# Performance work log

Measured on AMD Instinct MI355X. Metric: run time of the kernel, lower is better.

The kernel has to match this reference:

```python
import jax, jax.numpy as jnp
import numpy as np

T, D, H, E, K = 8192, 1024, 1024, 8, 2
N = T * K  # total dispatched rows


def setup_inputs() -> dict:
    key = jax.random.key(0)
    ks = jax.random.split(key, 12)
    s = 1.0 / np.sqrt(D)
    inp = {
        # uniform, contiguous per-expert segments: 2048 rows each
        'offsets': jnp.arange(E + 1, dtype=jnp.int64 if jax.config.jax_enable_x64 else jnp.int32) * (N // E),
        'jagged': jax.random.normal(ks[0], (T, D), jnp.float32),
        'weight': jax.random.normal(ks[1], (E, D, H), jnp.float32) * s,
        'bias': jax.random.normal(ks[2], (E, H), jnp.float32) * 0.02,
        'index': jax.random.randint(ks[3], (N,), 0, T),
        'weight_p': jax.random.normal(ks[4], (E, D, H), jnp.float32) * s,
        'weight_out': jax.random.normal(ks[5], (E, H, D), jnp.float32) * (1.0 / np.sqrt(H)),
        'reverse_index': jax.random.randint(ks[6], (T, K), 0, N),
        'gates': jax.random.uniform(ks[7], (N,), jnp.float32),
        'gates_index': jax.random.randint(ks[8], (T, K), 0, N),
        'bias_p': jax.random.normal(ks[9], (E, H), jnp.float32) * 0.02,
        'bias_out': jax.random.normal(ks[10], (E, D), jnp.float32) * 0.02,
    }
    return inp


def reference(offsets, jagged, weight, bias, index, weight_p, weight_out,
              reverse_index, gates, gates_index, bias_p, bias_out):
    # dispatch: gather token features into expert-sorted order  [N, D]
    x = jagged[index]
    n = x.shape[0]
    n_experts = weight.shape[0]
    # contiguous segment id per dispatched row
    expert_id = jnp.searchsorted(offsets, jnp.arange(n), side='right') - 1
    y = jnp.zeros((n, weight_out.shape[-1]), dtype=x.dtype)
    for e in range(n_experts):  # fixed small expert count
        m = (expert_id == e)[:, None].astype(x.dtype)
        xe = x * m
        g = xe @ weight[e] + bias[e]        # gate proj  [N, H]
        u = xe @ weight_p[e] + bias_p[e]    # up proj    [N, H]
        h = jax.nn.silu(g) * u              # SwiGLU
        y = y + (h @ weight_out[e] + bias_out[e]) * m
    # combine: gather K expert outputs per token, weight by gates  [T, D]
    gathered = y[reverse_index]             # [T, K, D]
    gv = gates[gates_index]                 # [T, K]
    return jnp.einsum('tkd,tk->td', gathered, gv)
```

## Files before the change

### kernel.cpp

```cpp
#include <hip/hip_runtime.h>
#include <hip/hip_bf16.h>

#define T_TOK 8192
#define DDIM 1024
#define HDIM 1024
#define NEXP 8
#define KTOP 2
#define NROWS (T_TOK * KTOP)

typedef __attribute__((ext_vector_type(8))) short bf16x8;
typedef __attribute__((ext_vector_type(8))) unsigned short u16x8;
typedef __attribute__((ext_vector_type(4))) float f32x4;

__device__ __forceinline__ unsigned short f2bf(float f) {
    unsigned u = __builtin_bit_cast(unsigned, f);
    u += 0x7fffu + ((u >> 16) & 1u);
    return (unsigned short)(u >> 16);
}
__device__ __forceinline__ float bf2f(unsigned short h) {
    return __builtin_bit_cast(float, (unsigned)h << 16);
}

__device__ __forceinline__ void gll16(const unsigned short* g, const unsigned short* l) {
    __builtin_amdgcn_global_load_lds(
        (const __attribute__((address_space(1))) unsigned int*)g,
        (__attribute__((address_space(3))) unsigned int*)l, 16, 0, 0);
}


__global__ __launch_bounds__(256) void cvt_bf16_k(const float* __restrict__ in,
                                                  unsigned short* __restrict__ out, int n4) {
    int i = blockIdx.x * 256 + threadIdx.x;
    if (i >= n4) return;
    float4 v = ((const float4*)in)[i];
    ushort4 o;
    o.x = f2bf(v.x); o.y = f2bf(v.y); o.z = f2bf(v.z); o.w = f2bf(v.w);
    ((ushort4*)out)[i] = o;
}

__global__ __launch_bounds__(256) void transpose_cast3_k(
    const float* __restrict__ w1, const float* __restrict__ w2,
    const float* __restrict__ w3, unsigned short* __restrict__ o1,
    unsigned short* __restrict__ o2, unsigned short* __restrict__ o3) {
    __shared__ float tile[64][65];
    int z = blockIdx.z;
    int which = z >> 3, m = z & 7;
    const float* src = (which == 0 ? w1 : which == 1 ? w2 : w3) + (size_t)m * DDIM * HDIM;
    unsigned short* dst = (which == 0 ? o1 : which == 1 ? o2 : o3) + (size_t)m * DDIM * HDIM;
    int c0 = blockIdx.x * 64, r0 = blockIdx.y * 64;
    int t = threadIdx.x;
    int rr = t >> 4;
    int cc = (t & 15) * 4;
#pragma unroll
    for (int p = 0; p < 4; ++p) {
        float4 v = *(const float4*)&src[(size_t)(r0 + rr + p * 16) * HDIM + c0 + cc];
        tile[rr + p * 16][cc]     = v.x;
        tile[rr + p * 16][cc + 1] = v.y;
        tile[rr + p * 16][cc + 2] = v.z;
        tile[rr + p * 16][cc + 3] = v.w;
    }
    __syncthreads();
    int rb = (t & 7) * 8;
    int oc = t >> 3;
#pragma unroll
    for (int q = 0; q < 2; ++q) {
        int c = oc + q * 32;
        u16x8 o;
#pragma unroll
        for (int j = 0; j < 8; ++j)
            o[j] = f2bf(tile[rb + j][c]);
        *(u16x8*)&dst[(size_t)(c0 + c) * DDIM + r0 + rb] = o;
    }
}


constexpr int BMk = 128, BNk = 128, BKk = 64;

template <int VARIANT>
__global__ __launch_bounds__(256, 4) void gemm128_k(
    const unsigned short* __restrict__ A, const int* __restrict__ rowidx, int lda,
    const unsigned short* __restrict__ Bt, const float* __restrict__ biasE,
    const unsigned short* __restrict__ Gin, unsigned short* __restrict__ Out,
    const int* __restrict__ offsets, int N, int K) {
    __shared__ __attribute__((aligned(16))) unsigned short lds[16384];

    const int nbn = N / BNk;
    int l = (blockIdx.x & 7) * 128 + (blockIdx.x >> 3);
    int brow = l / nbn, bcol = l % nbn;
    int row0 = brow * BMk, col0 = bcol * BNk;
    int e = 0;
    while (offsets[e + 1] <= row0) ++e;

    const unsigned short* Bte = Bt + (size_t)e * N * K;
    const float* bias = biasE + (size_t)e * N;

    int tid = threadIdx.x;
    int lane = tid & 63, wid = tid >> 6;
    int wr = wid >> 1, wc = wid & 1;
    int l15 = lane & 15, l4 = lane >> 4;

    int srow = lane >> 3;
    int c8 = ((lane & 7) ^ srow) * 8;
    const unsigned short* aS[4];
    const unsigned short* bS[4];
#pragma unroll
    for (int q = 0; q < 4; ++q) {
        int g = wid * 4 + q;
        int gr = row0 + g * 8 + srow;
        int ar = rowidx ? rowidx[gr] : gr;
        aS[q] = A + (size_t)ar * lda + c8;
        bS[q] = Bte + (size_t)(col0 + g * 8 + srow) * K + c8;
    }

    const char* LB = (const char*)lds;
    int arow = (wr * 64 + l15) * 128;
    int brw = (wc * 64 + l15) * 128;
    int cx = l15 & 7;
    int ch0 = (l4 ^ cx) * 16;
    int ch1 = ((4 + l4) ^ cx) * 16;

    f32x4 acc[4][4] = {};

#pragma unroll 1
    for (int t = 0; t < K / BKk; ++t) {
        int k0 = t * BKk;
#pragma unroll
        for (int q = 0; q < 4; ++q) {
            gll16(aS[q] + k0, lds + (wid * 4 + q) * 512);
            gll16(bS[q] + k0, lds + 8192 + (wid * 4 + q) * 512);
        }
        __syncthreads();
        bf16x8 fa[2][4], fb[2][4];
#pragma unroll
        for (int mi = 0; mi < 4; ++mi) {
            fa[0][mi] = *(const bf16x8*)(LB + arow + mi * 2048 + ch0);
            fa[1][mi] = *(const bf16x8*)(LB + arow + mi * 2048 + ch1);
        }
#pragma unroll
        for (int ni = 0; ni < 4; ++ni) {
            fb[0][ni] = *(const bf16x8*)(LB + 16384 + brw + ni * 2048 + ch0);
            fb[1][ni] = *(const bf16x8*)(LB + 16384 + brw + ni * 2048 + ch1);
        }
#pragma unroll
        for (int s = 0; s < 2; ++s)
#pragma unroll
            for (int mi = 0; mi < 4; ++mi)
#pragma unroll
                for (int ni = 0; ni < 4; ++ni)
                    acc[mi][ni] = __builtin_amdgcn_mfma_f32_16x16x32_bf16(
                        fa[s][mi], fb[s][ni], acc[mi][ni], 0, 0, 0);
        __syncthreads();
    }

    float bv[4];
#pragma unroll
    for (int ni = 0; ni < 4; ++ni)
        bv[ni] = bias[col0 + wc * 64 + ni * 16 + l15];

#pragma unroll
    for (int mi = 0; mi < 4; ++mi) {
        int orow_b = row0 + wr * 64 + mi * 16 + l4 * 4;
#pragma unroll
        for (int ni = 0; ni < 4; ++ni) {
            int ocol = col0 + wc * 64 + ni * 16 + l15;
#pragma unroll
            for (int q = 0; q < 4; ++q) {
                size_t oidx = (size_t)(orow_b + q) * N + ocol;
                float v = acc[mi][ni][q] + bv[ni];
                if (VARIANT == 1) {
                    float g = bf2f(Gin[oidx]);
                    float s = g / (1.0f + __expf(-g));
                    v = s * v;
                }
                Out[oidx] = f2bf(v);
            }
        }
    }
}


__global__ __launch_bounds__(256) void combine_k(
    const unsigned short* __restrict__ Y, const int* __restrict__ rev,
    const float* __restrict__ gates, const int* __restrict__ gidx,
    float* __restrict__ out) {
    int t = blockIdx.x;
    int r0 = rev[2 * t], r1 = rev[2 * t + 1];
    float g0 = gates[gidx[2 * t]], g1 = gates[gidx[2 * t + 1]];
    const unsigned short* y0 = Y + (size_t)r0 * DDIM;
    const unsigned short* y1 = Y + (size_t)r1 * DDIM;
    int d = threadIdx.x * 4;
    ushort4 a = *(const ushort4*)(y0 + d);
    ushort4 b = *(const ushort4*)(y1 + d);
    float4 r;
    r.x = g0 * bf2f(a.x) + g1 * bf2f(b.x);
    r.y = g0 * bf2f(a.y) + g1 * bf2f(b.y);
    r.z = g0 * bf2f(a.z) + g1 * bf2f(b.z);
    r.w = g0 * bf2f(a.w) + g1 * bf2f(b.w);
    *(float4*)(out + (size_t)t * DDIM + d) = r;
}


extern "C" void kernel_launch(void* const* d_in, const int* in_sizes, int n_in,
                              void* d_out, int out_size, void* d_ws, size_t ws_size,
                              hipStream_t stream) {
    const int* offsets = (const int*)d_in[0];
    const float* jagged = (const float*)d_in[1];
    const float* weight = (const float*)d_in[2];
    const float* bias = (const float*)d_in[3];
    const int* index = (const int*)d_in[4];
    const float* weight_p = (const float*)d_in[5];
    const float* weight_out = (const float*)d_in[6];
    const int* rev = (const int*)d_in[7];
    const float* gates = (const float*)d_in[8];
    const int* gidx = (const int*)d_in[9];
    const float* bias_p = (const float*)d_in[10];
    const float* bias_out = (const float*)d_in[11];
    float* out = (float*)d_out;

    char* w = (char*)d_ws;
    unsigned short* jag_bf = (unsigned short*)w; w += (size_t)T_TOK * DDIM * 2;
    unsigned short* W1t    = (unsigned short*)w; w += (size_t)NEXP * DDIM * HDIM * 2;
    unsigned short* Wpt    = (unsigned short*)w; w += (size_t)NEXP * DDIM * HDIM * 2;
    unsigned short* Wot    = (unsigned short*)w; w += (size_t)NEXP * HDIM * DDIM * 2;
    unsigned short* g_ws   = (unsigned short*)w; w += (size_t)NROWS * HDIM * 2;
    unsigned short* h_ws   = (unsigned short*)w; w += (size_t)NROWS * HDIM * 2;
    unsigned short* y_ws   = g_ws;

    cvt_bf16_k<<<(T_TOK * DDIM / 4 + 255) / 256, 256, 0, stream>>>(jagged, jag_bf, T_TOK * DDIM / 4);
    transpose_cast3_k<<<dim3(HDIM / 64, DDIM / 64, 3 * NEXP), 256, 0, stream>>>(
        weight, weight_p, weight_out, W1t, Wpt, Wot);

    const int grid = (NROWS / BMk) * (HDIM / BNk);

    gemm128_k<0><<<grid, 256, 0, stream>>>(jag_bf, index, DDIM, W1t, bias, nullptr, g_ws,
                                           offsets, HDIM, DDIM);
    gemm128_k<1><<<grid, 256, 0, stream>>>(jag_bf, index, DDIM, Wpt, bias_p, g_ws, h_ws,
                                           offsets, HDIM, DDIM);
    gemm128_k<0><<<grid, 256, 0, stream>>>(h_ws, nullptr, HDIM, Wot, bias_out, nullptr, y_ws,
                                           offsets, DDIM, HDIM);
    combine_k<<<T_TOK, 256, 0, stream>>>(y_ws, rev, gates, gidx, out);
}
```

Measured before the change: 171.7 us.

## Fuse gate and up projections into one dual-accumulator GEMM with SwiGLU epilogue

```diff
diff --git a/kernel.cpp b/kernel.cpp
--- a/kernel.cpp
+++ b/kernel.cpp
@@ -76,13 +76,13 @@
 
 constexpr int BMk = 128, BNk = 128, BKk = 64;
 
-template <int VARIANT>
-__global__ __launch_bounds__(256, 4) void gemm128_k(
-    const unsigned short* __restrict__ A, const int* __restrict__ rowidx, int lda,
-    const unsigned short* __restrict__ Bt, const float* __restrict__ biasE,
-    const unsigned short* __restrict__ Gin, unsigned short* __restrict__ Out,
-    const int* __restrict__ offsets, int N, int K) {
-    __shared__ __attribute__((aligned(16))) unsigned short lds[16384];
+__global__ __launch_bounds__(256, 3) void gemm128_fused_k(
+    const unsigned short* __restrict__ A, const int* __restrict__ rowidx,
+    const unsigned short* __restrict__ B1t, const unsigned short* __restrict__ B2t,
+    const float* __restrict__ b1E, const float* __restrict__ b2E,
+    unsigned short* __restrict__ Out, const int* __restrict__ offsets) {
+    const int N = HDIM, K = DDIM, lda = DDIM;
+    __shared__ __attribute__((aligned(16))) unsigned short lds[24576];
 
     const int nbn = N / BNk;
     int l = (blockIdx.x & 7) * 128 + (blockIdx.x >> 3);
@@ -91,8 +91,10 @@
     int e = 0;
     while (offsets[e + 1] <= row0) ++e;
 
-    const unsigned short* Bte = Bt + (size_t)e * N * K;
-    const float* bias = biasE + (size_t)e * N;
+    const unsigned short* B1e = B1t + (size_t)e * N * K;
+    const unsigned short* B2e = B2t + (size_t)e * N * K;
+    const float* b1 = b1E + (size_t)e * N;
+    const float* b2 = b2E + (size_t)e * N;
 
     int tid = threadIdx.x;
     int lane = tid & 63, wid = tid >> 6;
@@ -102,14 +104,15 @@
     int srow = lane >> 3;
     int c8 = ((lane & 7) ^ srow) * 8;
     const unsigned short* aS[4];
-    const unsigned short* bS[4];
+    const unsigned short* b1S[4];
+    const unsigned short* b2S[4];
 #pragma unroll
     for (int q = 0; q < 4; ++q) {
         int g = wid * 4 + q;
         int gr = row0 + g * 8 + srow;
-        int ar = rowidx ? rowidx[gr] : gr;
-        aS[q] = A + (size_t)ar * lda + c8;
-        bS[q] = Bte + (size_t)(col0 + g * 8 + srow) * K + c8;
+        aS[q]  = A + (size_t)rowidx[gr] * lda + c8;
+        b1S[q] = B1e + (size_t)(col0 + g * 8 + srow) * K + c8;
+        b2S[q] = B2e + (size_t)(col0 + g * 8 + srow) * K + c8;
     }
 
     const char* LB = (const char*)lds;
@@ -119,6 +122,109 @@
     int ch0 = (l4 ^ cx) * 16;
     int ch1 = ((4 + l4) ^ cx) * 16;
 
+    f32x4 acc1[4][4] = {};
+    f32x4 acc2[4][4] = {};
+
+#pragma unroll 1
+    for (int t = 0; t < K / BKk; ++t) {
+        int k0 = t * BKk;
+#pragma unroll
+        for (int q = 0; q < 4; ++q) {
+            gll16(aS[q] + k0,  lds + (wid * 4 + q) * 512);
+            gll16(b1S[q] + k0, lds + 8192 + (wid * 4 + q) * 512);
+            gll16(b2S[q] + k0, lds + 16384 + (wid * 4 + q) * 512);
+        }
+        __syncthreads();
+#pragma unroll
+        for (int s = 0; s < 2; ++s) {
+            int ch = s ? ch1 : ch0;
+            bf16x8 fa[4], fb1[4], fb2[4];
+#pragma unroll
+            for (int mi = 0; mi < 4; ++mi)
+                fa[mi] = *(const bf16x8*)(LB + arow + mi * 2048 + ch);
+#pragma unroll
+            for (int ni = 0; ni < 4; ++ni) {
+                fb1[ni] = *(const bf16x8*)(LB + 8192 * 2 + brw + ni * 2048 + ch);
+                fb2[ni] = *(const bf16x8*)(LB + 8192 * 4 + brw + ni * 2048 + ch);
+            }
+#pragma unroll
+            for (int mi = 0; mi < 4; ++mi)
+#pragma unroll
+                for (int ni = 0; ni < 4; ++ni) {
+                    acc1[mi][ni] = __builtin_amdgcn_mfma_f32_16x16x32_bf16(
+                        fa[mi], fb1[ni], acc1[mi][ni], 0, 0, 0);
+                    acc2[mi][ni] = __builtin_amdgcn_mfma_f32_16x16x32_bf16(
+                        fa[mi], fb2[ni], acc2[mi][ni], 0, 0, 0);
+                }
+        }
+        __syncthreads();
+    }
+
+    float bv1[4], bv2[4];
+#pragma unroll
+    for (int ni = 0; ni < 4; ++ni) {
+        int c = col0 + wc * 64 + ni * 16 + l15;
+        bv1[ni] = b1[c];
+        bv2[ni] = b2[c];
+    }
+
+#pragma unroll
+    for (int mi = 0; mi < 4; ++mi) {
+        int orow_b = row0 + wr * 64 + mi * 16 + l4 * 4;
+#pragma unroll
+        for (int ni = 0; ni < 4; ++ni) {
+            int ocol = col0 + wc * 64 + ni * 16 + l15;
+#pragma unroll
+            for (int q = 0; q < 4; ++q) {
+                float g = acc1[mi][ni][q] + bv1[ni];
+                float u = acc2[mi][ni][q] + bv2[ni];
+                float s = g / (1.0f + __expf(-g));
+                Out[(size_t)(orow_b + q) * N + ocol] = f2bf(s * u);
+            }
+        }
+    }
+}
+
+__global__ __launch_bounds__(256, 4) void gemm128_k(
+    const unsigned short* __restrict__ A, int lda,
+    const unsigned short* __restrict__ Bt, const float* __restrict__ biasE,
+    unsigned short* __restrict__ Out, const int* __restrict__ offsets,
+    int N, int K) {
+    __shared__ __attribute__((aligned(16))) unsigned short lds[16384];
+
+    const int nbn = N / BNk;
+    int l = (blockIdx.x & 7) * 128 + (blockIdx.x >> 3);
+    int brow = l / nbn, bcol = l % nbn;
+    int row0 = brow * BMk, col0 = bcol * BNk;
+    int e = 0;
+    while (offsets[e + 1] <= row0) ++e;
+
+    const unsigned short* Bte = Bt + (size_t)e * N * K;
+    const float* bias = biasE + (size_t)e * N;
+
+    int tid = threadIdx.x;
+    int lane = tid & 63, wid = tid >> 6;
+    int wr = wid >> 1, wc = wid & 1;
+    int l15 = lane & 15, l4 = lane >> 4;
+
+    int srow = lane >> 3;
+    int c8 = ((lane & 7) ^ srow) * 8;
+    const unsigned short* aS[4];
+    const unsigned short* bS[4];
+#pragma unroll
+    for (int q = 0; q < 4; ++q) {
+        int g = wid * 4 + q;
+        aS[q] = A + (size_t)(row0 + g * 8 + srow) * lda + c8;
+        bS[q] = Bte + (size_t)(col0 + g * 8 + srow) * K + c8;
+    }
+
+    const char* LB = (const char*)lds;
+    int arow = (wr * 64 + l15) * 128;
+    int brw = (wc * 64 + l15) * 128;
+    int cx = l15 & 7;
+    int ch0 = (l4 ^ cx) * 16;
+    int ch1 = ((4 + l4) ^ cx) * 16;
+
     f32x4 acc[4][4] = {};
 
 #pragma unroll 1
@@ -164,16 +270,8 @@
         for (int ni = 0; ni < 4; ++ni) {
             int ocol = col0 + wc * 64 + ni * 16 + l15;
 #pragma unroll
-            for (int q = 0; q < 4; ++q) {
-                size_t oidx = (size_t)(orow_b + q) * N + ocol;
-                float v = acc[mi][ni][q] + bv[ni];
-                if (VARIANT == 1) {
-                    float g = bf2f(Gin[oidx]);
-                    float s = g / (1.0f + __expf(-g));
-                    v = s * v;
-                }
-                Out[oidx] = f2bf(v);
-            }
+            for (int q = 0; q < 4; ++q)
+                Out[(size_t)(orow_b + q) * N + ocol] = f2bf(acc[mi][ni][q] + bv[ni]);
         }
     }
 }
@@ -222,9 +320,8 @@
     unsigned short* W1t    = (unsigned short*)w; w += (size_t)NEXP * DDIM * HDIM * 2;
     unsigned short* Wpt    = (unsigned short*)w; w += (size_t)NEXP * DDIM * HDIM * 2;
     unsigned short* Wot    = (unsigned short*)w; w += (size_t)NEXP * HDIM * DDIM * 2;
-    unsigned short* g_ws   = (unsigned short*)w; w += (size_t)NROWS * HDIM * 2;
     unsigned short* h_ws   = (unsigned short*)w; w += (size_t)NROWS * HDIM * 2;
-    unsigned short* y_ws   = g_ws;
+    unsigned short* y_ws   = (unsigned short*)w; w += (size_t)NROWS * DDIM * 2;
 
     cvt_bf16_k<<<(T_TOK * DDIM / 4 + 255) / 256, 256, 0, stream>>>(jagged, jag_bf, T_TOK * DDIM / 4);
     transpose_cast3_k<<<dim3(HDIM / 64, DDIM / 64, 3 * NEXP), 256, 0, stream>>>(
@@ -232,11 +329,9 @@
 
     const int grid = (NROWS / BMk) * (HDIM / BNk);
 
-    gemm128_k<0><<<grid, 256, 0, stream>>>(jag_bf, index, DDIM, W1t, bias, nullptr, g_ws,
-                                           offsets, HDIM, DDIM);
-    gemm128_k<1><<<grid, 256, 0, stream>>>(jag_bf, index, DDIM, Wpt, bias_p, g_ws, h_ws,
-                                           offsets, HDIM, DDIM);
-    gemm128_k<0><<<grid, 256, 0, stream>>>(h_ws, nullptr, HDIM, Wot, bias_out, nullptr, y_ws,
-                                           offsets, DDIM, HDIM);
+    gemm128_fused_k<<<grid, 256, 0, stream>>>(jag_bf, index, W1t, Wpt, bias, bias_p,
+                                              h_ws, offsets);
+    gemm128_k<<<grid, 256, 0, stream>>>(h_ws, HDIM, Wot, bias_out, y_ws,
+                                        offsets, DDIM, HDIM);
     combine_k<<<T_TOK, 256, 0, stream>>>(y_ws, rev, gates, gidx, out);
 }
```

New measurement: 331.5 us. +93.0%, slower.
